# Performance work log

Hardware: AMD Instinct MI355X
Metric: run time of the kernel (lower is better)

The kernel has to match this reference:

```python
import jax, jax.numpy as jnp
import numpy as np

N_HEADS = 8
EMBED = 512
N_LAYERS = 3
FF = 2048
IN_DIM = 256
BATCH = 32
GRAPH = 512
HEAD_DIM = EMBED // N_HEADS  # key_dim == val_dim == 64
BN_EPS = 1e-5


def setup_inputs() -> dict:
    key = jax.random.key(0)
    ks = jax.random.split(key, 16)
    u = lambda k, shape, fan: jax.random.uniform(k, shape, jnp.float32, -1.0, 1.0) / np.sqrt(fan)
    inp = {
        "x": jax.random.normal(ks[0], (BATCH, GRAPH, IN_DIM), jnp.float32),
        # init_embed Linear(graphsage_output_dim -> embed_dim)
        "W_init": u(ks[1], (IN_DIM, EMBED), IN_DIM),
        "b_init": u(ks[2], (EMBED,), IN_DIM),
        "eot": jnp.zeros((1, 1, EMBED), jnp.float32),  # end_of_token parameter
        # stacked per-layer MHA params (uniform(-1/sqrt(last_dim), ...) as in init_parameters)
        "Wq": u(ks[3], (N_LAYERS, N_HEADS, EMBED, HEAD_DIM), HEAD_DIM),
        "Wk": u(ks[4], (N_LAYERS, N_HEADS, EMBED, HEAD_DIM), HEAD_DIM),
        "Wv": u(ks[5], (N_LAYERS, N_HEADS, EMBED, HEAD_DIM), HEAD_DIM),
        "Wo": u(ks[6], (N_LAYERS, N_HEADS, HEAD_DIM, EMBED), EMBED),
        # BatchNorm affine params (BN1 after attention skip, BN2 after FFN skip)
        "bn1_g": jnp.ones((N_LAYERS, EMBED), jnp.float32),
        "bn1_b": jnp.zeros((N_LAYERS, EMBED), jnp.float32),
        "W1": u(ks[7], (N_LAYERS, EMBED, FF), EMBED),
        "b1": u(ks[8], (N_LAYERS, FF), EMBED),
        "W2": u(ks[9], (N_LAYERS, FF, EMBED), FF),
        "b2": u(ks[10], (N_LAYERS, EMBED), FF),
        "bn2_g": jnp.ones((N_LAYERS, EMBED), jnp.float32),
        "bn2_b": jnp.zeros((N_LAYERS, EMBED), jnp.float32),
    }
    return inp


def _mha(h, Wq, Wk, Wv, Wo):
    # h: [b, n, d]; Wq/Wk/Wv: [H, d, k]; Wo: [H, k, d]
    scale = float(HEAD_DIM) ** -0.5
    Q = jnp.einsum("bnd,hdk->hbnk", h, Wq)
    K = jnp.einsum("bnd,hdk->hbnk", h, Wk)
    V = jnp.einsum("bnd,hdk->hbnk", h, Wv)
    attn = jax.nn.softmax(jnp.einsum("hbqk,hbnk->hbqn", Q, K) * scale, axis=-1)
    heads = jnp.einsum("hbqn,hbnk->hbqk", attn, V)
    return jnp.einsum("hbqk,hkd->bqd", heads, Wo)


def _batchnorm(h, gamma, beta):
    # BatchNorm1d in train mode over flattened (batch*seq, embed)
    hf = h.reshape(-1, h.shape[-1])
    m = hf.mean(axis=0)
    v = hf.var(axis=0)  # biased variance, as in torch BN normalization
    return ((hf - m) * jax.lax.rsqrt(v + BN_EPS) * gamma + beta).reshape(h.shape)


def reference(x, W_init, b_init, eot, Wq, Wk, Wv, Wo, bn1_g, bn1_b, W1, b1, W2, b2, bn2_g, bn2_b):
    h = x @ W_init + b_init                                   # [b, n, d]
    eot_b = jnp.broadcast_to(eot, (h.shape[0], 1, h.shape[-1]))
    h = jnp.concatenate([h, eot_b], axis=1)                   # [b, n+1, d]
    for i in range(N_LAYERS):
        h = _batchnorm(h + _mha(h, Wq[i], Wk[i], Wv[i], Wo[i]), bn1_g[i], bn1_b[i])
        ff = jax.nn.relu(h @ W1[i] + b1[i]) @ W2[i] + b2[i]
        h = _batchnorm(h + ff, bn2_g[i], bn2_b[i])
    return h
```

## Files before the change

### kernel.cpp

```cpp
#include <hip/hip_runtime.h>
#include <stdint.h>

typedef unsigned short u16;
typedef __attribute__((ext_vector_type(8))) short bfrag;
typedef __attribute__((ext_vector_type(4))) float f32x4;

#define MFMA16(a,b,c) __builtin_amdgcn_mfma_f32_16x16x32_bf16(a,b,c,0,0,0)

__device__ __forceinline__ u16 f2b(float f){
  union { float f; uint32_t u; } v; v.f = f;
  uint32_t r = v.u + 0x7FFFu + ((v.u >> 16) & 1u);
  return (u16)(r >> 16);
}
__device__ __forceinline__ uint32_t cvtpk(float lo, float hi){
  uint32_t r; asm("v_cvt_pk_bf16_f32 %0, %1, %2" : "=v"(r) : "v"(lo), "v"(hi)); return r;
}

typedef const __attribute__((address_space(1))) unsigned int* gas_t;
typedef __attribute__((address_space(3))) unsigned int* las_t;
__device__ __forceinline__ void async16(const u16* g, u16* l){
  __builtin_amdgcn_global_load_lds((gas_t)g, (las_t)l, 16, 0, 0);
}

__global__ __launch_bounds__(256) void cvt_x_k(const float* __restrict__ x, u16* __restrict__ o, int n){
  int i = blockIdx.x*256 + threadIdx.x;
  if (i < n) o[i] = f2b(x[i]);
}
__global__ __launch_bounds__(256) void eot_k(const float* __restrict__ eot, float* __restrict__ hF, u16* __restrict__ hbf){
  int i = blockIdx.x*256 + threadIdx.x;
  int b = i >> 9, d = i & 511;
  float v = eot[d];
  size_t idx = ((size_t)b*513 + 512)*512 + d;
  hF[idx] = v; hbf[idx] = f2b(v);
}

template<typename T>
__global__ __launch_bounds__(256) void trans_k(const T* __restrict__ src, u16* __restrict__ dst,
    int R, int C, int SS, int DS, int div, size_t srcA, size_t srcB, size_t dstA, size_t dstB)
{
  __shared__ u16 tile[64][72];
  int s = blockIdx.z;
  const T* sp = src + (size_t)(s/div)*srcA + (size_t)(s%div)*srcB;
  u16* dp = dst + (size_t)(s/div)*dstA + (size_t)(s%div)*dstB;
  int r0 = blockIdx.x*64, c0 = blockIdx.y*64;
  int t = threadIdx.x;
  int tr = t>>2, tc = (t&3)*16;
  int rr = r0+tr; if (rr >= R) rr = R-1;
  const T* p = sp + (size_t)rr*SS + c0 + tc;
  u16 bv[16];
  if constexpr (sizeof(T)==4) {
    float4 a = *(const float4*)p, b = *(const float4*)(p+4),
           c = *(const float4*)(p+8), d = *(const float4*)(p+12);
    float f[16] = {a.x,a.y,a.z,a.w,b.x,b.y,b.z,b.w,c.x,c.y,c.z,c.w,d.x,d.y,d.z,d.w};
    #pragma unroll
    for (int i=0;i<16;i++) bv[i] = f2b(f[i]);
  } else {
    *(uint4*)&bv[0] = ((const uint4*)p)[0];
    *(uint4*)&bv[8] = ((const uint4*)p)[1];
  }
  *(uint4*)&tile[tr][tc]   = *(uint4*)&bv[0];
  *(uint4*)&tile[tr][tc+8] = *(uint4*)&bv[8];
  __syncthreads();
  int oc = t>>2, orr = (t&3)*16;
  u16 ov[16];
  #pragma unroll
  for (int i=0;i<16;i++) ov[i] = tile[orr+i][oc];
  u16* q = dp + (size_t)(c0+oc)*DS + r0 + orr;
  if (r0 + 64 <= R) {
    *(uint4*)q     = *(uint4*)&ov[0];
    *(uint4*)(q+8) = *(uint4*)&ov[8];
  } else {
    #pragma unroll
    for (int i=0;i<16;i++){
      int rg = r0 + orr + i;
      if (rg < DS) q[i] = (rg < R) ? ov[i] : (u16)0;
    }
  }
}

template<bool BIAS,bool RELU,bool SKIP,bool OUTF,bool OUTB,bool REMAP>
__global__ __launch_bounds__(256,2) void gemm_k(
    const u16* __restrict__ A, const u16* __restrict__ BT,
    const float* __restrict__ bias, const float* __restrict__ skip,
    float* __restrict__ outF, u16* __restrict__ outB,
    int M, int N, int K)
{
  __shared__ u16 Ash[128*64];
  __shared__ u16 Bsh[128*64];
  const int tid = threadIdx.x;
  const int lane = tid & 63, wv = tid >> 6;
  const int mt = blockIdx.x, nt = blockIdx.y;
  const int wrow = (wv >> 1) << 6, wcol = (wv & 1) << 6;
  const int g = lane >> 4, ci = lane & 15;

  f32x4 acc[4][4];
  #pragma unroll
  for (int i=0;i<4;i++)
    #pragma unroll
    for (int j=0;j<4;j++) acc[i][j] = (f32x4){0.f,0.f,0.f,0.f};

  int aofs[4][2], bofs[4][2];
  #pragma unroll
  for (int mi=0;mi<4;mi++){
    int rr = wrow + mi*16 + ci;
    int cc = wcol + mi*16 + ci;
    #pragma unroll
    for (int kh=0;kh<2;kh++){
      aofs[mi][kh] = rr*64 + ((((kh<<2)|g) ^ (rr&7))<<3);
      bofs[mi][kh] = cc*64 + ((((kh<<2)|g) ^ (cc&7))<<3);
    }
  }
  const u16* ga[4]; const u16* gb[4];
  #pragma unroll
  for (int q=0;q<4;q++){
    int row = q*32 + (tid>>3);
    int sc  = (tid&7) ^ (row&7);
    int arow = mt*128 + row; if (arow >= M) arow = M-1;
    int brow = nt*128 + row;
    ga[q] = A  + (size_t)arow*K + sc*8;
    gb[q] = BT + (size_t)brow*K + sc*8;
  }
  u16* la = Ash + tid*8;
  u16* lb = Bsh + tid*8;

  for (int kt = 0; kt < K; kt += 64){
    #pragma unroll
    for (int q=0;q<4;q++) async16(ga[q] + kt, la + q*2048);
    #pragma unroll
    for (int q=0;q<4;q++) async16(gb[q] + kt, lb + q*2048);
    __syncthreads();
    #pragma unroll
    for (int kh=0;kh<2;kh++){
      bfrag a[4], b[4];
      #pragma unroll
      for (int mi=0;mi<4;mi++) a[mi] = *(const bfrag*)&Ash[aofs[mi][kh]];
      #pragma unroll
      for (int ni=0;ni<4;ni++) b[ni] = *(const bfrag*)&Bsh[bofs[ni][kh]];
      #pragma unroll
      for (int mi=0;mi<4;mi++)
        #pragma unroll
        for (int ni=0;ni<4;ni++)
          acc[mi][ni] = MFMA16(a[mi], b[ni], acc[mi][ni]);
    }
    __syncthreads();
  }

  #pragma unroll
  for (int mi=0;mi<4;mi++){
    #pragma unroll
    for (int r=0;r<4;r++){
      int gm = mt*128 + wrow + mi*16 + g*4 + r;
      if (gm >= M) continue;
      size_t orow = REMAP ? (size_t)(gm + (gm >> 9)) : (size_t)gm;
      #pragma unroll
      for (int ni=0;ni<4;ni++){
        int gn = nt*128 + wcol + ni*16 + ci;
        float v = acc[mi][ni][r];
        if (BIAS) v += bias[gn];
        if (SKIP) v += skip[(size_t)gm*N + gn];
        if (RELU) v = fmaxf(v, 0.f);
        if (OUTF) outF[orow*N + gn] = v;
        if (OUTB) outB[orow*N + gn] = f2b(v);
      }
    }
  }
}

#define LOG2E_SC 0.1803368801f
__global__ __launch_bounds__(256) void attn_k(const u16* __restrict__ qkv, const u16* __restrict__ Vt,
                                              u16* __restrict__ heads)
{
  __shared__ u16 P_lds[4][16*72];
  const int wv = threadIdx.x >> 6;
  const int qt = blockIdx.x*4 + wv;
  if (qt > 32) return;
  const int b = blockIdx.y, hh = blockIdx.z;
  const int lane = threadIdx.x & 63;
  const int g = lane >> 4, ci = lane & 15;
  u16* P_l = P_lds[wv];

  const size_t rowb = (size_t)b * 513;
  int q = qt*16 + ci; int qr = q < 513 ? q : 512;
  const u16* qp = qkv + (rowb + qr)*1536 + hh*64 + g*8;
  bfrag aq0 = *(const bfrag*)qp;
  bfrag aq1 = *(const bfrag*)(qp + 32);

  const u16* kbase = qkv + rowb*1536 + 512 + hh*64;
  const u16* vbase = Vt + (size_t)(b*8 + hh)*33280;

  f32x4 hacc[4];
  #pragma unroll
  for (int dt=0;dt<4;dt++) hacc[dt] = (f32x4){0.f,0.f,0.f,0.f};
  float mrun = -1e30f, srun = 0.f;

  for (int np = 0; np < 9; ++np){
    const int n0 = np*64;
    const bool tail = (np == 8);
    float p_[4][4];
    #pragma unroll
    for (int t=0;t<4;t++){
      int n = n0 + t*16 + ci; if (n > 512) n = 512;
      const u16* kp = kbase + (size_t)n*1536;
      bfrag k0 = *(const bfrag*)(kp + g*8);
      bfrag k1 = *(const bfrag*)(kp + 32 + g*8);
      f32x4 z = (f32x4){0.f,0.f,0.f,0.f};
      z = MFMA16(k0, aq0, z);
      z = MFMA16(k1, aq1, z);
      #pragma unroll
      for (int r=0;r<4;r++) p_[t][r] = z[r]*LOG2E_SC;
    }
    if (tail){
      #pragma unroll
      for (int t=0;t<4;t++)
        #pragma unroll
        for (int r=0;r<4;r++)
          if (n0 + t*16 + g*4 + r >= 513) p_[t][r] = -1e30f;
    }
    bfrag vf[4][2];
    #pragma unroll
    for (int dt=0;dt<4;dt++){
      const u16* vr = vbase + (size_t)(dt*16 + ci)*520;
      #pragma unroll
      for (int kh=0;kh<2;kh++){
        int nv = tail ? 512 : (n0 + kh*32 + g*8);
        vf[dt][kh] = *(const bfrag*)(vr + nv);
      }
    }
    float pm = p_[0][0];
    #pragma unroll
    for (int t=0;t<4;t++)
      #pragma unroll
      for (int r=0;r<4;r++) pm = fmaxf(pm, p_[t][r]);
    pm = fmaxf(pm, __shfl_xor(pm, 16));
    pm = fmaxf(pm, __shfl_xor(pm, 32));
    float mn = fmaxf(mrun, pm);
    float f = __builtin_exp2f(mrun - mn);
    mrun = mn;
    float ps = 0.f;
    #pragma unroll
    for (int t=0;t<4;t++)
      #pragma unroll
      for (int r=0;r<4;r++){ p_[t][r] = __builtin_exp2f(p_[t][r] - mn); ps += p_[t][r]; }
    ps += __shfl_xor(ps, 16);
    ps += __shfl_xor(ps, 32);
    srun = srun*f + ps;
    #pragma unroll
    for (int dt=0;dt<4;dt++){
      hacc[dt][0]*=f; hacc[dt][1]*=f; hacc[dt][2]*=f; hacc[dt][3]*=f;
    }
    #pragma unroll
    for (int t=0;t<4;t++){
      uint2 w2; w2.x = cvtpk(p_[t][0], p_[t][1]); w2.y = cvtpk(p_[t][2], p_[t][3]);
      *(uint2*)&P_l[ci*72 + t*16 + g*4] = w2;
    }
    bfrag pb0 = *(const bfrag*)&P_l[ci*72 + g*8];
    bfrag pb1 = *(const bfrag*)&P_l[ci*72 + 32 + g*8];
    #pragma unroll
    for (int dt=0;dt<4;dt++){
      hacc[dt] = MFMA16(vf[dt][0], pb0, hacc[dt]);
      hacc[dt] = MFMA16(vf[dt][1], pb1, hacc[dt]);
    }
  }
  float rs = 1.0f / srun;
  #pragma unroll
  for (int dt=0;dt<4;dt++)
    #pragma unroll
    for (int r=0;r<4;r++)
      P_l[ci*72 + dt*16 + g*4 + r] = f2b(hacc[dt][r]*rs);
  bfrag o0 = *(const bfrag*)&P_l[ci*72 + g*8];
  bfrag o1 = *(const bfrag*)&P_l[ci*72 + 32 + g*8];
  if (qt*16 + ci < 513){
    u16* hp = heads + (rowb + qt*16 + ci)*512 + hh*64 + g*8;
    *(bfrag*)hp = o0;
    *(bfrag*)(hp + 32) = o1;
  }
}

#define NB 1026
__global__ __launch_bounds__(256) void bn_stats_k(const float* __restrict__ in, float* __restrict__ p1, float* __restrict__ p2){
  int blk = blockIdx.x, t = threadIdx.x;
  int c4 = t & 127, rh = t >> 7;
  float4 s = {0,0,0,0}, qq = {0,0,0,0};
  for (int i = rh; i < 32; i += 2){
    float4 v = ((const float4*)in)[(size_t)(blk*32 + i)*128 + c4];
    s.x += v.x; s.y += v.y; s.z += v.z; s.w += v.w;
    qq.x += v.x*v.x; qq.y += v.y*v.y; qq.z += v.z*v.z; qq.w += v.w*v.w;
  }
  size_t base = (size_t)(c4*4)*NB + blk*2 + rh;
  p1[base] = s.x; p1[base+NB] = s.y; p1[base+2*NB] = s.z; p1[base+3*NB] = s.w;
  p2[base] = qq.x; p2[base+NB] = qq.y; p2[base+2*NB] = qq.z; p2[base+3*NB] = qq.w;
}
__global__ __launch_bounds__(256) void bn_fin_k(const float* __restrict__ p1, const float* __restrict__ p2,
                                               const float* __restrict__ gamma, const float* __restrict__ beta,
                                               float2* __restrict__ sc){
  const int c = blockIdx.x;
  const int t = threadIdx.x;
  float S = 0.f, Q = 0.f;
  for (int i = t; i < NB; i += 256){
    S += p1[(size_t)c*NB + i];
    Q += p2[(size_t)c*NB + i];
  }
  #pragma unroll
  for (int m = 1; m < 64; m <<= 1){
    S += __shfl_xor(S, m);
    Q += __shfl_xor(Q, m);
  }
  __shared__ float sS[4], sQ[4];
  int wv = t >> 6, lane = t & 63;
  if (lane == 0){ sS[wv] = S; sQ[wv] = Q; }
  __syncthreads();
  if (t == 0){
    float Sa = (sS[0]+sS[1]) + (sS[2]+sS[3]);
    float Qa = (sQ[0]+sQ[1]) + (sQ[2]+sQ[3]);
    const float invM = 1.0f/16416.0f;
    float mean = Sa*invM;
    float var  = Qa*invM - mean*mean;
    float scl  = gamma[c] * rsqrtf(var + 1e-5f);
    sc[c] = make_float2(scl, beta[c] - mean*scl);
  }
}
__global__ __launch_bounds__(256) void bn_apply_k(const float* __restrict__ in, const float2* __restrict__ sc,
                                                  float* __restrict__ outF, u16* __restrict__ outB){
  const int n4 = 16416*512/4;
  for (int i = blockIdx.x*256 + threadIdx.x; i < n4; i += gridDim.x*256){
    float4 v = ((const float4*)in)[i];
    int c0 = (i << 2) & 511;
    float2 a = sc[c0], b = sc[c0+1], c = sc[c0+2], d = sc[c0+3];
    v.x = v.x*a.x + a.y; v.y = v.y*b.x + b.y; v.z = v.z*c.x + c.y; v.w = v.w*d.x + d.y;
    ((float4*)outF)[i] = v;
    ushort4 u; u.x=f2b(v.x); u.y=f2b(v.y); u.z=f2b(v.z); u.w=f2b(v.w);
    ((ushort4*)outB)[i] = u;
  }
}

static inline size_t alignup(size_t x){ return (x + 255) & ~(size_t)255; }

extern "C" void kernel_launch(void* const* d_in, const int* in_sizes, int n_in,
                              void* d_out, int out_size, void* d_ws, size_t ws_size,
                              hipStream_t stream)
{
  (void)in_sizes; (void)n_in; (void)out_size; (void)ws_size;
  const float* x      = (const float*)d_in[0];
  const float* W_init = (const float*)d_in[1];
  const float* b_init = (const float*)d_in[2];
  const float* eot    = (const float*)d_in[3];
  const float* Wq     = (const float*)d_in[4];
  const float* Wk     = (const float*)d_in[5];
  const float* Wv     = (const float*)d_in[6];
  const float* Wo     = (const float*)d_in[7];
  const float* bn1g   = (const float*)d_in[8];
  const float* bn1b   = (const float*)d_in[9];
  const float* W1     = (const float*)d_in[10];
  const float* b1     = (const float*)d_in[11];
  const float* W2     = (const float*)d_in[12];
  const float* b2     = (const float*)d_in[13];
  const float* bn2g   = (const float*)d_in[14];
  const float* bn2b   = (const float*)d_in[15];

  char* ws = (char*)d_ws;
  size_t o = 0;
  u16*    hbf    = (u16*)  (ws + o); o += alignup(16416ull*512*2);
  float*  hF     = (float*)(ws + o); o += alignup(16416ull*512*4);
  float*  bufB   = (float*)(ws + o); o += alignup(16416ull*512*4);
  u16*    heads  = (u16*)  (ws + o); o += alignup(16416ull*512*2);
  u16*    big    = (u16*)  (ws + o); o += alignup(16416ull*2048*2);
  u16*    winitT = (u16*)  (ws + o); o += alignup(512ull*256*2);
  u16*    wqkvT  = (u16*)  (ws + o); o += alignup(3ull*1536*512*2);
  u16*    woT    = (u16*)  (ws + o); o += alignup(3ull*512*512*2);
  u16*    w1T    = (u16*)  (ws + o); o += alignup(3ull*2048*512*2);
  u16*    w2T    = (u16*)  (ws + o); o += alignup(3ull*512*2048*2);
  float*  p1     = (float*)(ws + o); o += alignup(512ull*NB*4);
  float*  p2     = (float*)(ws + o); o += alignup(512ull*NB*4);
  float2* scv    = (float2*)(ws + o); o += alignup(512*8);
  u16* xbf = big; u16* qkv = big; u16* ffb = big;
  u16* VtB = (u16*)bufB;

  cvt_x_k<<<16384,256,0,stream>>>(x, xbf, 16384*256);
  trans_k<float><<<dim3(4,8,1),   256,0,stream>>>(W_init, winitT, 256, 512, 512, 256, 1, 131072, 0, 0, 0);
  trans_k<float><<<dim3(8,1,24),  256,0,stream>>>(Wq, wqkvT,            512, 64, 64, 512, 8, 262144, 32768, 786432, 32768);
  trans_k<float><<<dim3(8,1,24),  256,0,stream>>>(Wk, wqkvT + 262144,   512, 64, 64, 512, 8, 262144, 32768, 786432, 32768);
  trans_k<float><<<dim3(8,1,24),  256,0,stream>>>(Wv, wqkvT + 524288,   512, 64, 64, 512, 8, 262144, 32768, 786432, 32768);
  trans_k<float><<<dim3(1,8,24),  256,0,stream>>>(Wo, woT,  64, 512, 512, 512, 8, 262144, 32768, 262144, 64);
  trans_k<float><<<dim3(8,32,3),  256,0,stream>>>(W1, w1T,  512, 2048, 2048, 512, 1, 1048576, 0, 1048576, 0);
  trans_k<float><<<dim3(32,8,3),  256,0,stream>>>(W2, w2T,  2048, 512, 512, 2048, 1, 1048576, 0, 1048576, 0);

  gemm_k<true,false,false,true,true,true><<<dim3(128,4),256,0,stream>>>(
      xbf, winitT, b_init, nullptr, hF, hbf, 16384, 512, 256);
  eot_k<<<64,256,0,stream>>>(eot, hF, hbf);

  for (int l = 0; l < 3; ++l){
    gemm_k<false,false,false,false,true,false><<<dim3(129,12),256,0,stream>>>(
        hbf, wqkvT + (size_t)l*1536*512, nullptr, nullptr, nullptr, qkv, 16416, 1536, 512);
    trans_k<u16><<<dim3(9,1,256),256,0,stream>>>(qkv + 1024, VtB, 513, 64, 1536, 520, 8, 787968, 64, 266240, 33280);
    attn_k<<<dim3(9,32,8),256,0,stream>>>(qkv, VtB, heads);
    gemm_k<false,false,true,true,false,false><<<dim3(129,4),256,0,stream>>>(
        heads, woT + (size_t)l*512*512, nullptr, hF, bufB, nullptr, 16416, 512, 512);
    bn_stats_k<<<513,256,0,stream>>>(bufB, p1, p2);
    bn_fin_k  <<<512,256,0,stream>>>(p1, p2, bn1g + l*512, bn1b + l*512, scv);
    bn_apply_k<<<2048,256,0,stream>>>(bufB, scv, hF, hbf);
    gemm_k<true,true,false,false,true,false><<<dim3(129,16),256,0,stream>>>(
        hbf, w1T + (size_t)l*2048*512, b1 + l*2048, nullptr, nullptr, ffb, 16416, 2048, 512);
    gemm_k<true,false,true,true,false,false><<<dim3(129,4),256,0,stream>>>(
        ffb, w2T + (size_t)l*512*2048, b2 + l*512, hF, bufB, nullptr, 16416, 512, 2048);
    bn_stats_k<<<513,256,0,stream>>>(bufB, p1, p2);
    bn_fin_k  <<<512,256,0,stream>>>(p1, p2, bn2g + l*512, bn2b + l*512, scv);
    bn_apply_k<<<2048,256,0,stream>>>(bufB, scv, (l==2) ? (float*)d_out : hF, hbf);
  }
}
```

Baseline: 1.266 ms.

## Stage GEMM epilogue through LDS for vectorized stores; prefetch K tiles in attention

The GEMM epilogue now writes each wave's accumulator fragment into shared memory (reusing the A tile buffer) and reads it back row-contiguous, so bias, skip and output accesses become float4/ushort4 vector operations instead of scattered scalar ones. The attention kernel double-buffers K fragments in registers, loading the next 64-key block while computing the current one, and fully unrolls the key loop to hide global load latency. The trade-offs are extra LDS traffic in the epilogue and higher register pressure in attention from the second K buffer and the unrolling.

```diff
diff --git a/kernel.cpp b/kernel.cpp
--- a/kernel.cpp
+++ b/kernel.cpp
@@ -85,8 +85,8 @@
     float* __restrict__ outF, u16* __restrict__ outB,
     int M, int N, int K)
 {
-  __shared__ u16 Ash[128*64];
-  __shared__ u16 Bsh[128*64];
+  __shared__ __align__(16) u16 Ash[128*64];
+  __shared__ __align__(16) u16 Bsh[128*64];
   const int tid = threadIdx.x;
   const int lane = tid & 63, wv = tid >> 6;
   const int mt = blockIdx.x, nt = blockIdx.y;
@@ -145,22 +145,39 @@
     __syncthreads();
   }
 
+  float* Cw = ((float*)Ash) + wv*1024;
   #pragma unroll
   for (int mi=0;mi<4;mi++){
     #pragma unroll
-    for (int r=0;r<4;r++){
-      int gm = mt*128 + wrow + mi*16 + g*4 + r;
-      if (gm >= M) continue;
-      size_t orow = REMAP ? (size_t)(gm + (gm >> 9)) : (size_t)gm;
-      #pragma unroll
-      for (int ni=0;ni<4;ni++){
-        int gn = nt*128 + wcol + ni*16 + ci;
-        float v = acc[mi][ni][r];
-        if (BIAS) v += bias[gn];
-        if (SKIP) v += skip[(size_t)gm*N + gn];
-        if (RELU) v = fmaxf(v, 0.f);
-        if (OUTF) outF[orow*N + gn] = v;
-        if (OUTB) outB[orow*N + gn] = f2b(v);
+    for (int ni=0;ni<4;ni++)
+      #pragma unroll
+      for (int r=0;r<4;r++)
+        Cw[(g*4+r)*64 + ni*16 + ci] = acc[mi][ni][r];
+    #pragma unroll
+    for (int it=0; it<4; ++it){
+      int chunk = it*64 + lane;
+      int row = chunk >> 4, c4 = (chunk & 15) << 2;
+      int gm = mt*128 + wrow + mi*16 + row;
+      if (gm < M){
+        float4 v = *(float4*)&Cw[row*64 + c4];
+        int gn = nt*128 + wcol + c4;
+        size_t orow = REMAP ? (size_t)(gm + (gm >> 9)) : (size_t)gm;
+        if (BIAS){
+          float4 bv = *(const float4*)&bias[gn];
+          v.x += bv.x; v.y += bv.y; v.z += bv.z; v.w += bv.w;
+        }
+        if (SKIP){
+          float4 sv = *(const float4*)&skip[(size_t)gm*N + gn];
+          v.x += sv.x; v.y += sv.y; v.z += sv.z; v.w += sv.w;
+        }
+        if (RELU){
+          v.x = fmaxf(v.x,0.f); v.y = fmaxf(v.y,0.f); v.z = fmaxf(v.z,0.f); v.w = fmaxf(v.w,0.f);
+        }
+        if (OUTF) *(float4*)&outF[orow*N + gn] = v;
+        if (OUTB){
+          ushort4 u; u.x=f2b(v.x); u.y=f2b(v.y); u.z=f2b(v.z); u.w=f2b(v.w);
+          *(ushort4*)&outB[orow*N + gn] = u;
+        }
       }
     }
   }
@@ -193,19 +210,35 @@
   for (int dt=0;dt<4;dt++) hacc[dt] = (f32x4){0.f,0.f,0.f,0.f};
   float mrun = -1e30f, srun = 0.f;
 
+  bfrag kbuf[2][4][2];
+  #pragma unroll
+  for (int t=0;t<4;t++){
+    const u16* kp = kbase + (size_t)(t*16 + ci)*1536;
+    kbuf[0][t][0] = *(const bfrag*)(kp + g*8);
+    kbuf[0][t][1] = *(const bfrag*)(kp + 32 + g*8);
+  }
+
+  #pragma unroll
   for (int np = 0; np < 9; ++np){
+    const int cur = np & 1, nxt = cur ^ 1;
+    if (np < 8){
+      const int n1 = (np+1)*64;
+      #pragma unroll
+      for (int t=0;t<4;t++){
+        int n = n1 + t*16 + ci; if (n > 512) n = 512;
+        const u16* kp = kbase + (size_t)n*1536;
+        kbuf[nxt][t][0] = *(const bfrag*)(kp + g*8);
+        kbuf[nxt][t][1] = *(const bfrag*)(kp + 32 + g*8);
+      }
+    }
     const int n0 = np*64;
     const bool tail = (np == 8);
     float p_[4][4];
     #pragma unroll
     for (int t=0;t<4;t++){
-      int n = n0 + t*16 + ci; if (n > 512) n = 512;
-      const u16* kp = kbase + (size_t)n*1536;
-      bfrag k0 = *(const bfrag*)(kp + g*8);
-      bfrag k1 = *(const bfrag*)(kp + 32 + g*8);
       f32x4 z = (f32x4){0.f,0.f,0.f,0.f};
-      z = MFMA16(k0, aq0, z);
-      z = MFMA16(k1, aq1, z);
+      z = MFMA16(kbuf[cur][t][0], aq0, z);
+      z = MFMA16(kbuf[cur][t][1], aq1, z);
       #pragma unroll
       for (int r=0;r<4;r++) p_[t][r] = z[r]*LOG2E_SC;
     }
```

After: 1.282 ms. About the same (+1.3%).
